# Kernel optimization log

Hardware: AMD Instinct MI355X
Metric: run time of the kernel (lower is better)

Reference implementation:

```python
import math
import jax, jax.numpy as jnp
import numpy as np

B, T, D_MODEL, H, D = 2, 1024, 1024, 16, 64
NUM_LEVELS = int(math.ceil(math.log2(T + 1))) + 1  # 12 for max_seq_len=1024


def _fenwick_level(idx):
    return (idx & -idx).bit_length() - 1


def build_fenwick_masks(T, num_levels):
    """NumPy replica of the torch build_fenwick_masks; returns [L, T, T] float32."""
    j_to_nodes = {}
    for j in range(1, T + 1):
        nodes = []
        idx = j
        while idx <= T:
            nodes.append((idx, _fenwick_level(idx)))
            idx += idx & -idx
        j_to_nodes[j] = nodes
    t_to_query_nodes = {}
    for t in range(1, T + 1):
        s = set()
        idx = t
        while idx > 0:
            s.add(idx)
            idx -= idx & -idx
        t_to_query_nodes[t] = s
    masks = np.zeros((num_levels, T, T), dtype=np.float32)
    for t in range(1, T + 1):
        qn = t_to_query_nodes[t]
        for j in range(1, t + 1):
            for node_idx, node_level in j_to_nodes[j]:
                if node_idx in qn:
                    masks[min(node_level, num_levels - 1), t - 1, j - 1] = 1.0
                    break
    return masks


def setup_inputs() -> dict:
    key = jax.random.key(0)
    ks = jax.random.split(key, 8)
    s = 0.02
    return {
        "x": jax.random.normal(ks[0], (B, T, D_MODEL), jnp.float32),
        "qw": jax.random.normal(ks[1], (D_MODEL, H * D), jnp.float32) * s,
        "qb": jnp.zeros((H * D,), jnp.float32),
        "kw": jax.random.normal(ks[2], (D_MODEL, H * D), jnp.float32) * s,
        "kb": jnp.zeros((H * D,), jnp.float32),
        "vw": jax.random.normal(ks[3], (D_MODEL, H * D), jnp.float32) * s,
        "vb": jnp.zeros((H * D,), jnp.float32),
        "lw": jax.random.normal(ks[4], (D_MODEL, H * NUM_LEVELS), jnp.float32) * s,
        "lb": jnp.zeros((H * NUM_LEVELS,), jnp.float32),
        "ow": jax.random.normal(ks[5], (H * D, D_MODEL), jnp.float32) * s,
        "ob": jnp.zeros((D_MODEL,), jnp.float32),
        "level_masks": jnp.asarray(build_fenwick_masks(T, NUM_LEVELS)),
    }


def reference(x, qw, qb, kw, kb, vw, vb, lw, lb, ow, ob, level_masks):
    b, t, _ = x.shape
    phi = lambda a: jax.nn.elu(a) + 1.0  # ELU+1 feature map
    # projections -> [B, H, T, D]
    Q = (x @ qw + qb).reshape(b, t, H, D).transpose(0, 2, 1, 3)
    K = (x @ kw + kb).reshape(b, t, H, D).transpose(0, 2, 1, 3)
    V = (x @ vw + vb).reshape(b, t, H, D).transpose(0, 2, 1, 3)
    Qp, Kp = phi(Q), phi(K)
    # per-level mixing weights: [B, H, T, L]
    logits = (x @ lw + lb).reshape(b, t, H, NUM_LEVELS).transpose(0, 2, 1, 3)
    w = jax.nn.softmax(logits, axis=-1)
    # scores are level-independent in the original; compute once
    S = jnp.einsum('bhid,bhjd->bhij', Qp, Kp)
    # sum_l w_l * mask_l folded into one weighted mask: [B, H, T, T]
    Mw = jnp.einsum('bhil,lij->bhij', w, level_masks)
    Sm = S * Mw
    num = jnp.einsum('bhij,bhjd->bhid', Sm, V)
    den = jnp.maximum(jnp.sum(Sm, axis=-1, keepdims=True), 1e-6)
    out = (num / den).transpose(0, 2, 1, 3).reshape(b, t, H * D)
    return out @ ow + ob
```

## Files before the change

### kernel.cpp

```cpp
#include <hip/hip_runtime.h>
#include <math.h>

typedef __bf16 bf16;
typedef __attribute__((ext_vector_type(8))) __bf16 bf16x8;
typedef __attribute__((ext_vector_type(4))) float f32x4;

#define B_SZ 2
#define T_SZ 1024
#define DM_SZ 1024
#define H_SZ 16
#define D_SZ 64
#define L_SZ 12
#define M_ROWS 2048
#define N_FUSED 3264

__device__ __forceinline__ f32x4 mfma_16x16x32(bf16x8 a, bf16x8 b, f32x4 c) {
  return __builtin_amdgcn_mfma_f32_16x16x32_bf16(a, b, c, 0, 0, 0);
}

__global__ __launch_bounds__(256) void k_cast(const float* __restrict__ in,
                                              bf16* __restrict__ out) {
  const int idx = blockIdx.x * 256 + threadIdx.x;
  const float* p = in + (size_t)idx * 8;
  f32x4 a = *(const f32x4*)p;
  f32x4 b = *(const f32x4*)(p + 4);
  bf16x8 o;
#pragma unroll
  for (int e = 0; e < 4; ++e) { o[e] = (bf16)a[e]; o[e + 4] = (bf16)b[e]; }
  *(bf16x8*)(out + (size_t)idx * 8) = o;
}

__global__ __launch_bounds__(256) void k_transpose4(
    const float* __restrict__ in0, bf16* __restrict__ out0,
    const float* __restrict__ in1, bf16* __restrict__ out1,
    const float* __restrict__ in2, bf16* __restrict__ out2,
    const float* __restrict__ in3, bf16* __restrict__ out3, int R, int C) {
  __shared__ __align__(16) bf16 tile[64][66];
  const float* in = blockIdx.z == 0 ? in0 : blockIdx.z == 1 ? in1 : blockIdx.z == 2 ? in2 : in3;
  bf16* out = blockIdx.z == 0 ? out0 : blockIdx.z == 1 ? out1 : blockIdx.z == 2 ? out2 : out3;
  const int tc = blockIdx.x * 64;
  const int tr = blockIdx.y * 64;
  const int t = threadIdx.x;
  const int r = t >> 2;
  const int c4 = (t & 3) << 4;
  const float* src = in + (size_t)(tr + r) * C + tc + c4;
  f32x4 f0 = *(const f32x4*)(src);
  f32x4 f1 = *(const f32x4*)(src + 4);
  f32x4 f2 = *(const f32x4*)(src + 8);
  f32x4 f3 = *(const f32x4*)(src + 12);
#pragma unroll
  for (int e = 0; e < 4; ++e) {
    tile[r][c4 + e]      = (bf16)f0[e];
    tile[r][c4 + 4 + e]  = (bf16)f1[e];
    tile[r][c4 + 8 + e]  = (bf16)f2[e];
    tile[r][c4 + 12 + e] = (bf16)f3[e];
  }
  __syncthreads();
  bf16x8 w0, w1;
#pragma unroll
  for (int e = 0; e < 8; ++e) { w0[e] = tile[c4 + e][r]; w1[e] = tile[c4 + 8 + e][r]; }
  bf16* dst = out + (size_t)(tc + r) * R + tr + c4;
  *(bf16x8*)(dst) = w0;
  *(bf16x8*)(dst + 8) = w1;
}

__global__ __launch_bounds__(256) void k_vtrans(const bf16* __restrict__ V,
                                                bf16* __restrict__ VTg) {
  __shared__ __align__(16) bf16 tile[64][66];
  const int tt = blockIdx.x;
  const int bh = blockIdx.y;
  const int b = bh >> 4, h = bh & 15;
  const int t0 = tt * 64;
  const int t = threadIdx.x;
  const int r = t >> 2;
  const int c4 = (t & 3) << 4;
  const bf16* src = V + (size_t)(b * T_SZ + t0 + r) * DM_SZ + h * 64 + c4;
  bf16x8 v0 = *(const bf16x8*)(src);
  bf16x8 v1 = *(const bf16x8*)(src + 8);
#pragma unroll
  for (int e = 0; e < 8; ++e) { tile[r][c4 + e] = v0[e]; tile[r][c4 + 8 + e] = v1[e]; }
  __syncthreads();
  bf16x8 w0, w1;
#pragma unroll
  for (int e = 0; e < 8; ++e) { w0[e] = tile[c4 + e][r]; w1[e] = tile[c4 + 8 + e][r]; }
  bf16* dst = VTg + ((size_t)bh * 64 + r) * T_SZ + t0 + c4;
  *(bf16x8*)(dst) = w0;
  *(bf16x8*)(dst + 8) = w1;
}

__global__ __launch_bounds__(256) void k_gemm_qkvl(
    const bf16* __restrict__ A, const bf16* __restrict__ Wt,
    const float* __restrict__ qb, const float* __restrict__ kb,
    const float* __restrict__ vb, const float* __restrict__ lb,
    bf16* __restrict__ Qp, bf16* __restrict__ Kp, bf16* __restrict__ V,
    float* __restrict__ logit) {
  __shared__ __align__(16) bf16 As[128][80];
  __shared__ __align__(16) bf16 Bs[64][80];
  const int nb = blockIdx.x * 64;
  const int mb = blockIdx.y * 128;
  const int t = threadIdx.x;
  const int wv = t >> 6;
  const int lane = t & 63;
  const int l16 = lane & 15;
  const int quad = lane >> 4;
  const int m0 = wv * 32;

  const int ar = t >> 1;
  const int ak = (t & 1) << 5;
  const int br = t >> 2;
  const int bk = (t & 3) << 4;

  const f32x4 zero4 = {0.f, 0.f, 0.f, 0.f};
  f32x4 acc[2][4];
#pragma unroll
  for (int i = 0; i < 2; ++i)
#pragma unroll
    for (int j = 0; j < 4; ++j) acc[i][j] = zero4;

  for (int k0 = 0; k0 < DM_SZ; k0 += 64) {
    const bf16* apg = A + (size_t)(mb + ar) * DM_SZ + k0 + ak;
    bf16x8 a0 = *(const bf16x8*)(apg);
    bf16x8 a1 = *(const bf16x8*)(apg + 8);
    bf16x8 a2 = *(const bf16x8*)(apg + 16);
    bf16x8 a3 = *(const bf16x8*)(apg + 24);
    const bf16* bpg = Wt + (size_t)(nb + br) * DM_SZ + k0 + bk;
    bf16x8 b0 = *(const bf16x8*)(bpg);
    bf16x8 b1 = *(const bf16x8*)(bpg + 8);
    __syncthreads();
    *(bf16x8*)&As[ar][ak] = a0;
    *(bf16x8*)&As[ar][ak + 8] = a1;
    *(bf16x8*)&As[ar][ak + 16] = a2;
    *(bf16x8*)&As[ar][ak + 24] = a3;
    *(bf16x8*)&Bs[br][bk] = b0;
    *(bf16x8*)&Bs[br][bk + 8] = b1;
    __syncthreads();
#pragma unroll
    for (int ks = 0; ks < 2; ++ks) {
      bf16x8 af0 = *(const bf16x8*)&As[m0 + l16][ks * 32 + quad * 8];
      bf16x8 af1 = *(const bf16x8*)&As[m0 + 16 + l16][ks * 32 + quad * 8];
#pragma unroll
      for (int tn = 0; tn < 4; ++tn) {
        bf16x8 bfr = *(const bf16x8*)&Bs[tn * 16 + l16][ks * 32 + quad * 8];
        acc[0][tn] = mfma_16x16x32(af0, bfr, acc[0][tn]);
        acc[1][tn] = mfma_16x16x32(af1, bfr, acc[1][tn]);
      }
    }
  }

  const int seg = nb >> 10;
  const int colseg0 = nb - (seg << 10);
  const float* bias = seg == 0 ? qb : seg == 1 ? kb : seg == 2 ? vb : lb;
  bf16* outb = seg == 0 ? Qp : seg == 1 ? Kp : V;

#pragma unroll
  for (int mi = 0; mi < 2; ++mi) {
#pragma unroll
    for (int tn = 0; tn < 4; ++tn) {
      const int col = colseg0 + tn * 16 + l16;
      const float bv = bias[col];
#pragma unroll
      for (int r = 0; r < 4; ++r) {
        const int row = mb + m0 + mi * 16 + quad * 4 + r;
        float v = acc[mi][tn][r] + bv;
        if (seg == 3) {
          logit[(size_t)row * (H_SZ * L_SZ) + col] = v;
        } else {
          if (seg < 2) v = (v > 0.f) ? (v + 1.f) : __expf(v);
          outb[(size_t)row * DM_SZ + col] = (bf16)v;
        }
      }
    }
  }
}

__global__ __launch_bounds__(256) void k_softmax12(float* __restrict__ lg, int n) {
  const int idx = blockIdx.x * 256 + threadIdx.x;
  if (idx >= n) return;
  float* p = lg + (size_t)idx * L_SZ;
  float m = p[0];
#pragma unroll
  for (int l = 1; l < L_SZ; ++l) m = fmaxf(m, p[l]);
  float e[L_SZ], s = 0.f;
#pragma unroll
  for (int l = 0; l < L_SZ; ++l) { e[l] = __expf(p[l] - m); s += e[l]; }
  const float inv = 1.f / s;
#pragma unroll
  for (int l = 0; l < L_SZ; ++l) p[l] = e[l] * inv;
}

__global__ __launch_bounds__(256) void k_attn(const bf16* __restrict__ Qp,
                                              const bf16* __restrict__ Kp,
                                              const bf16* __restrict__ VTg,
                                              const float* __restrict__ W,
                                              bf16* __restrict__ O) {
  __shared__ __align__(16) bf16 Ks[64][80];
  __shared__ __align__(16) bf16 VTs[64][80];
  __shared__ __align__(16) bf16 Pl[4][16][80];
  __shared__ float Ws[64 * L_SZ];

  const int idx = blockIdx.x;
  const int s = idx >> 5;
  const int bh = idx & 31;
  const int it = (s < 8) ? (15 - s) : (s - 8);
  const int b = bh >> 4;
  const int h = bh & 15;
  const int i0 = it * 64;
  const int t = threadIdx.x;
  const int wv = t >> 6;
  const int lane = t & 63;
  const int l16 = lane & 15;
  const int quad = lane >> 4;
  const int m0 = wv * 16;

  const size_t base_bt = (size_t)b * T_SZ;

  const bf16* qptr = Qp + (base_bt + i0 + m0 + l16) * DM_SZ + h * 64 + quad * 8;
  const bf16x8 aq0 = *(const bf16x8*)(qptr);
  const bf16x8 aq1 = *(const bf16x8*)(qptr + 32);

  {
    const int f = t * 3;
#pragma unroll
    for (int u = 0; u < 3; ++u) {
      const int ff = f + u;
      const int il = ff / L_SZ, l = ff % L_SZ;
      Ws[ff] = W[(base_bt + i0 + il) * (H_SZ * L_SZ) + h * L_SZ + l];
    }
  }

  const f32x4 zero4 = {0.f, 0.f, 0.f, 0.f};
  f32x4 accn[4];
#pragma unroll
  for (int tn = 0; tn < 4; ++tn) accn[tn] = zero4;
  float den[4] = {0.f, 0.f, 0.f, 0.f};

  const int sr = t >> 2;
  const int sc = (t & 3) << 4;

  const bf16* vtrow = VTg + ((size_t)bh * 64 + sr) * T_SZ;

  for (int jt = 0; jt <= it; ++jt) {
    const int j0 = jt * 64;
    const bf16* kpg = Kp + (base_bt + j0 + sr) * DM_SZ + h * 64 + sc;
    bf16x8 k0v = *(const bf16x8*)(kpg);
    bf16x8 k1v = *(const bf16x8*)(kpg + 8);
    const bf16* vpg = vtrow + j0 + sc;
    bf16x8 v0v = *(const bf16x8*)(vpg);
    bf16x8 v1v = *(const bf16x8*)(vpg + 8);
    __syncthreads();
    *(bf16x8*)&Ks[sr][sc] = k0v;
    *(bf16x8*)&Ks[sr][sc + 8] = k1v;
    *(bf16x8*)&VTs[sr][sc] = v0v;
    *(bf16x8*)&VTs[sr][sc + 8] = v1v;
    __syncthreads();

    f32x4 sacc[4];
#pragma unroll
    for (int tn = 0; tn < 4; ++tn) {
      sacc[tn] = zero4;
      bf16x8 bk0 = *(const bf16x8*)&Ks[tn * 16 + l16][quad * 8];
      bf16x8 bk1 = *(const bf16x8*)&Ks[tn * 16 + l16][32 + quad * 8];
      sacc[tn] = mfma_16x16x32(aq0, bk0, sacc[tn]);
      sacc[tn] = mfma_16x16x32(aq1, bk1, sacc[tn]);
    }

#pragma unroll
    for (int tn = 0; tn < 4; ++tn) {
#pragma unroll
      for (int r = 0; r < 4; ++r) {
        const int il = m0 + quad * 4 + r;
        const int ig = i0 + il;
        const int jg = j0 + tn * 16 + l16;
        float p = 0.f;
        if (jg <= ig) {
          const int lvl = 31 - __clz((unsigned)((ig + 1) ^ jg));
          p = sacc[tn][r] * Ws[il * L_SZ + lvl];
        }
        den[r] += p;
        Pl[wv][quad * 4 + r][(tn * 16 + l16) ^ (quad << 4)] = (bf16)p;
      }
    }

#pragma unroll
    for (int ks = 0; ks < 2; ++ks) {
      bf16x8 apf = *(const bf16x8*)&Pl[wv][l16][(ks * 32 + quad * 8) ^ ((l16 >> 2) << 4)];
#pragma unroll
      for (int tn = 0; tn < 4; ++tn) {
        bf16x8 bvf = *(const bf16x8*)&VTs[tn * 16 + l16][ks * 32 + quad * 8];
        accn[tn] = mfma_16x16x32(apf, bvf, accn[tn]);
      }
    }
  }

#pragma unroll
  for (int r = 0; r < 4; ++r) {
    float d = den[r];
    d += __shfl_xor(d, 1, 64);
    d += __shfl_xor(d, 2, 64);
    d += __shfl_xor(d, 4, 64);
    d += __shfl_xor(d, 8, 64);
    den[r] = fmaxf(d, 1e-6f);
  }

#pragma unroll
  for (int tn = 0; tn < 4; ++tn) {
#pragma unroll
    for (int r = 0; r < 4; ++r) {
      const int il = m0 + quad * 4 + r;
      O[(base_bt + i0 + il) * DM_SZ + h * 64 + tn * 16 + l16] =
          (bf16)(accn[tn][r] / den[r]);
    }
  }
}

__global__ __launch_bounds__(256) void k_gemm_out(const bf16* __restrict__ A,
                                                  const bf16* __restrict__ Wt,
                                                  const float* __restrict__ bias,
                                                  float* __restrict__ out) {
  __shared__ __align__(16) bf16 As[64][80];
  __shared__ __align__(16) bf16 Bs[64][80];
  const int nb = blockIdx.x * 64;
  const int mb = blockIdx.y * 64;
  const int t = threadIdx.x;
  const int wv = t >> 6;
  const int lane = t & 63;
  const int l16 = lane & 15;
  const int quad = lane >> 4;

  const int sr = t >> 2;
  const int sc = (t & 3) << 4;

  const f32x4 zero4 = {0.f, 0.f, 0.f, 0.f};
  f32x4 acc[4];
#pragma unroll
  for (int j = 0; j < 4; ++j) acc[j] = zero4;

  for (int k0 = 0; k0 < DM_SZ; k0 += 64) {
    const bf16* apg = A + (size_t)(mb + sr) * DM_SZ + k0 + sc;
    bf16x8 a0 = *(const bf16x8*)(apg);
    bf16x8 a1 = *(const bf16x8*)(apg + 8);
    const bf16* bpg = Wt + (size_t)(nb + sr) * DM_SZ + k0 + sc;
    bf16x8 b0 = *(const bf16x8*)(bpg);
    bf16x8 b1 = *(const bf16x8*)(bpg + 8);
    __syncthreads();
    *(bf16x8*)&As[sr][sc] = a0;
    *(bf16x8*)&As[sr][sc + 8] = a1;
    *(bf16x8*)&Bs[sr][sc] = b0;
    *(bf16x8*)&Bs[sr][sc + 8] = b1;
    __syncthreads();
#pragma unroll
    for (int ks = 0; ks < 2; ++ks) {
      bf16x8 af = *(const bf16x8*)&As[wv * 16 + l16][ks * 32 + quad * 8];
#pragma unroll
      for (int tn = 0; tn < 4; ++tn) {
        bf16x8 bfr = *(const bf16x8*)&Bs[tn * 16 + l16][ks * 32 + quad * 8];
        acc[tn] = mfma_16x16x32(af, bfr, acc[tn]);
      }
    }
  }
#pragma unroll
  for (int tn = 0; tn < 4; ++tn) {
    const int col = nb + tn * 16 + l16;
    const float bv = bias[col];
#pragma unroll
    for (int r = 0; r < 4; ++r) {
      const int row = mb + wv * 16 + quad * 4 + r;
      out[(size_t)row * DM_SZ + col] = acc[tn][r] + bv;
    }
  }
}

extern "C" void kernel_launch(void* const* d_in, const int* in_sizes, int n_in,
                              void* d_out, int out_size, void* d_ws, size_t ws_size,
                              hipStream_t stream) {
  (void)in_sizes; (void)n_in; (void)out_size; (void)ws_size;
  const float* x  = (const float*)d_in[0];
  const float* qw = (const float*)d_in[1];
  const float* qb = (const float*)d_in[2];
  const float* kw = (const float*)d_in[3];
  const float* kb = (const float*)d_in[4];
  const float* vw = (const float*)d_in[5];
  const float* vb = (const float*)d_in[6];
  const float* lw = (const float*)d_in[7];
  const float* lb = (const float*)d_in[8];
  const float* ow = (const float*)d_in[9];
  const float* ob = (const float*)d_in[10];

  char* ws = (char*)d_ws;
  size_t off = 0;
  auto alloc = [&](size_t bytes) -> char* {
    char* p = ws + off;
    off += (bytes + 255) & ~(size_t)255;
    return p;
  };
  bf16* xb     = (bf16*)alloc((size_t)M_ROWS * DM_SZ * 2);
  bf16* wqkvlT = (bf16*)alloc((size_t)N_FUSED * DM_SZ * 2);
  bf16* owT    = (bf16*)alloc((size_t)DM_SZ * DM_SZ * 2);
  bf16* Qp     = (bf16*)alloc((size_t)M_ROWS * DM_SZ * 2);
  bf16* Kpb    = (bf16*)alloc((size_t)M_ROWS * DM_SZ * 2);
  bf16* Vb     = (bf16*)alloc((size_t)M_ROWS * DM_SZ * 2);
  bf16* VTg    = (bf16*)alloc((size_t)M_ROWS * DM_SZ * 2);
  bf16* attn   = (bf16*)alloc((size_t)M_ROWS * DM_SZ * 2);
  float* logit = (float*)alloc((size_t)M_ROWS * H_SZ * L_SZ * 4);

  const dim3 blk(256);
  k_cast<<<dim3(M_ROWS * DM_SZ / 8 / 256), blk, 0, stream>>>(x, xb);
  k_transpose4<<<dim3(16, 16, 4), blk, 0, stream>>>(
      qw, wqkvlT, kw, wqkvlT + (size_t)1024 * DM_SZ, vw, wqkvlT + (size_t)2048 * DM_SZ,
      ow, owT, DM_SZ, DM_SZ);
  k_transpose4<<<dim3(3, 16, 1), blk, 0, stream>>>(
      lw, wqkvlT + (size_t)3072 * DM_SZ, lw, nullptr, lw, nullptr, lw, nullptr,
      DM_SZ, H_SZ * L_SZ);

  k_gemm_qkvl<<<dim3(N_FUSED / 64, M_ROWS / 128), blk, 0, stream>>>(
      xb, wqkvlT, qb, kb, vb, lb, Qp, Kpb, Vb, logit);

  k_softmax12<<<dim3((M_ROWS * H_SZ) / 256), blk, 0, stream>>>(logit, M_ROWS * H_SZ);
  k_vtrans<<<dim3(T_SZ / 64, B_SZ * H_SZ), blk, 0, stream>>>(Vb, VTg);

  k_attn<<<dim3((T_SZ / 64) * B_SZ * H_SZ), blk, 0, stream>>>(Qp, Kpb, VTg, logit, attn);

  k_gemm_out<<<dim3(DM_SZ / 64, M_ROWS / 64), blk, 0, stream>>>(attn, owT, ob, (float*)d_out);
}
```

Baseline: 202.0 us.

## Use 128-wide direct-to-LDS GEMMs, split logit GEMM, fuse softmax into attention

Replaces the QKV and output projection GEMMs with a templated 128-column-tile GEMM. It loads tiles straight into LDS through global_load_lds, which removes register staging and the padded LDS layout. The logit projection moves to its own small GEMM, and the level softmax is computed inside the attention kernel, so the separate softmax launch is dropped. The weight transposes are merged into a single launch. The unpadded LDS layout may cause bank conflicts, and each block still loads once per k-step with no double buffering.

```diff
diff --git a/kernel.cpp b/kernel.cpp
--- a/kernel.cpp
+++ b/kernel.cpp
@@ -12,10 +12,16 @@
 #define D_SZ 64
 #define L_SZ 12
 #define M_ROWS 2048
-#define N_FUSED 3264
+#define N_QKV 3072
 
 __device__ __forceinline__ f32x4 mfma_16x16x32(bf16x8 a, bf16x8 b, f32x4 c) {
   return __builtin_amdgcn_mfma_f32_16x16x32_bf16(a, b, c, 0, 0, 0);
+}
+
+__device__ __forceinline__ void gload_lds16(const bf16* g, bf16* l) {
+  __builtin_amdgcn_global_load_lds((const __attribute__((address_space(1))) void*)g,
+                                   (__attribute__((address_space(3))) void*)l,
+                                   16, 0, 0);
 }
 
 __global__ __launch_bounds__(256) void k_cast(const float* __restrict__ in,
@@ -30,14 +36,21 @@
   *(bf16x8*)(out + (size_t)idx * 8) = o;
 }
 
-__global__ __launch_bounds__(256) void k_transpose4(
+__global__ __launch_bounds__(256) void k_transpose5(
     const float* __restrict__ in0, bf16* __restrict__ out0,
     const float* __restrict__ in1, bf16* __restrict__ out1,
     const float* __restrict__ in2, bf16* __restrict__ out2,
-    const float* __restrict__ in3, bf16* __restrict__ out3, int R, int C) {
+    const float* __restrict__ in3, bf16* __restrict__ out3,
+    const float* __restrict__ in4, bf16* __restrict__ out4) {
   __shared__ __align__(16) bf16 tile[64][66];
-  const float* in = blockIdx.z == 0 ? in0 : blockIdx.z == 1 ? in1 : blockIdx.z == 2 ? in2 : in3;
-  bf16* out = blockIdx.z == 0 ? out0 : blockIdx.z == 1 ? out1 : blockIdx.z == 2 ? out2 : out3;
+  const int z = blockIdx.z;
+  const float* in; bf16* out; int C = 1024;
+  if (z == 0)      { in = in0; out = out0; }
+  else if (z == 1) { in = in1; out = out1; }
+  else if (z == 2) { in = in2; out = out2; }
+  else if (z == 3) { in = in3; out = out3; }
+  else             { in = in4; out = out4; C = 192; if (blockIdx.x >= 3) return; }
+  const int R = 1024;
   const int tc = blockIdx.x * 64;
   const int tr = blockIdx.y * 64;
   const int t = threadIdx.x;
@@ -88,12 +101,105 @@
   *(bf16x8*)(dst + 8) = w1;
 }
 
-__global__ __launch_bounds__(256) void k_gemm_qkvl(
+template <int TM, int EPI>
+__global__ __launch_bounds__(256) void k_gemm128(
     const bf16* __restrict__ A, const bf16* __restrict__ Wt,
     const float* __restrict__ qb, const float* __restrict__ kb,
-    const float* __restrict__ vb, const float* __restrict__ lb,
+    const float* __restrict__ vb,
     bf16* __restrict__ Qp, bf16* __restrict__ Kp, bf16* __restrict__ V,
-    float* __restrict__ logit) {
+    float* __restrict__ outF) {
+  constexpr int MI = TM / 32;
+  __shared__ __align__(16) bf16 As[TM * 64];
+  __shared__ __align__(16) bf16 Bs[128 * 64];
+  const int nb = blockIdx.x * 128;
+  const int mb = blockIdx.y * TM;
+  const int t = threadIdx.x;
+  const int wv = t >> 6;
+  const int lane = t & 63;
+  const int l16 = lane & 15;
+  const int quad = lane >> 4;
+  const int wm = (wv & 1) * (TM / 2);
+  const int wn = (wv >> 1) * 64;
+
+  const int trow = t >> 3;
+  const int tcol = (t & 7) * 8;
+
+  const f32x4 zero4 = {0.f, 0.f, 0.f, 0.f};
+  f32x4 acc[MI][4];
+#pragma unroll
+  for (int i = 0; i < MI; ++i)
+#pragma unroll
+    for (int j = 0; j < 4; ++j) acc[i][j] = zero4;
+
+  const bf16* ag = A + (size_t)(mb + trow) * DM_SZ + tcol;
+  const bf16* bg = Wt + (size_t)(nb + trow) * DM_SZ + tcol;
+
+  for (int k0 = 0; k0 < DM_SZ; k0 += 64) {
+    __syncthreads();
+#pragma unroll
+    for (int i = 0; i < MI; ++i)
+      gload_lds16(ag + (size_t)i * 32 * DM_SZ + k0, As + i * 2048 + t * 8);
+#pragma unroll
+    for (int i = 0; i < 4; ++i)
+      gload_lds16(bg + (size_t)i * 32 * DM_SZ + k0, Bs + i * 2048 + t * 8);
+    __syncthreads();
+#pragma unroll
+    for (int ks = 0; ks < 2; ++ks) {
+      bf16x8 af[MI];
+#pragma unroll
+      for (int mi = 0; mi < MI; ++mi)
+        af[mi] = *(const bf16x8*)(As + (wm + mi * 16 + l16) * 64 + ks * 32 + quad * 8);
+#pragma unroll
+      for (int ni = 0; ni < 4; ++ni) {
+        bf16x8 bfr = *(const bf16x8*)(Bs + (wn + ni * 16 + l16) * 64 + ks * 32 + quad * 8);
+#pragma unroll
+        for (int mi = 0; mi < MI; ++mi)
+          acc[mi][ni] = mfma_16x16x32(af[mi], bfr, acc[mi][ni]);
+      }
+    }
+  }
+
+  if (EPI == 0) {
+    const int seg = nb >> 10;
+    const int c0 = (nb & 1023) + wn;
+    const float* bias = seg == 0 ? qb : seg == 1 ? kb : vb;
+    bf16* outp = seg == 0 ? Qp : seg == 1 ? Kp : V;
+#pragma unroll
+    for (int ni = 0; ni < 4; ++ni) {
+      const int col = c0 + ni * 16 + l16;
+      const float bv = bias[col];
+#pragma unroll
+      for (int mi = 0; mi < MI; ++mi) {
+#pragma unroll
+        for (int r = 0; r < 4; ++r) {
+          const int row = mb + wm + mi * 16 + quad * 4 + r;
+          float v = acc[mi][ni][r] + bv;
+          if (seg < 2) v = (v > 0.f) ? (v + 1.f) : __expf(v);
+          outp[(size_t)row * DM_SZ + col] = (bf16)v;
+        }
+      }
+    }
+  } else {
+#pragma unroll
+    for (int ni = 0; ni < 4; ++ni) {
+      const int col = nb + wn + ni * 16 + l16;
+      const float bv = qb[col];
+#pragma unroll
+      for (int mi = 0; mi < MI; ++mi) {
+#pragma unroll
+        for (int r = 0; r < 4; ++r) {
+          const int row = mb + wm + mi * 16 + quad * 4 + r;
+          outF[(size_t)row * DM_SZ + col] = acc[mi][ni][r] + bv;
+        }
+      }
+    }
+  }
+}
+
+__global__ __launch_bounds__(256) void k_gemm_logit(const bf16* __restrict__ A,
+                                                    const bf16* __restrict__ Wt,
+                                                    const float* __restrict__ lb,
+                                                    float* __restrict__ logit) {
   __shared__ __align__(16) bf16 As[128][80];
   __shared__ __align__(16) bf16 Bs[64][80];
   const int nb = blockIdx.x * 64;
@@ -146,52 +252,25 @@
       }
     }
   }
-
-  const int seg = nb >> 10;
-  const int colseg0 = nb - (seg << 10);
-  const float* bias = seg == 0 ? qb : seg == 1 ? kb : seg == 2 ? vb : lb;
-  bf16* outb = seg == 0 ? Qp : seg == 1 ? Kp : V;
-
 #pragma unroll
   for (int mi = 0; mi < 2; ++mi) {
 #pragma unroll
     for (int tn = 0; tn < 4; ++tn) {
-      const int col = colseg0 + tn * 16 + l16;
-      const float bv = bias[col];
+      const int col = nb + tn * 16 + l16;
+      const float bv = lb[col];
 #pragma unroll
       for (int r = 0; r < 4; ++r) {
         const int row = mb + m0 + mi * 16 + quad * 4 + r;
-        float v = acc[mi][tn][r] + bv;
-        if (seg == 3) {
-          logit[(size_t)row * (H_SZ * L_SZ) + col] = v;
-        } else {
-          if (seg < 2) v = (v > 0.f) ? (v + 1.f) : __expf(v);
-          outb[(size_t)row * DM_SZ + col] = (bf16)v;
-        }
-      }
-    }
-  }
-}
-
-__global__ __launch_bounds__(256) void k_softmax12(float* __restrict__ lg, int n) {
-  const int idx = blockIdx.x * 256 + threadIdx.x;
-  if (idx >= n) return;
-  float* p = lg + (size_t)idx * L_SZ;
-  float m = p[0];
-#pragma unroll
-  for (int l = 1; l < L_SZ; ++l) m = fmaxf(m, p[l]);
-  float e[L_SZ], s = 0.f;
-#pragma unroll
-  for (int l = 0; l < L_SZ; ++l) { e[l] = __expf(p[l] - m); s += e[l]; }
-  const float inv = 1.f / s;
-#pragma unroll
-  for (int l = 0; l < L_SZ; ++l) p[l] = e[l] * inv;
+        logit[(size_t)row * (H_SZ * L_SZ) + col] = acc[mi][tn][r] + bv;
+      }
+    }
+  }
 }
 
 __global__ __launch_bounds__(256) void k_attn(const bf16* __restrict__ Qp,
                                               const bf16* __restrict__ Kp,
                                               const bf16* __restrict__ VTg,
-                                              const float* __restrict__ W,
+                                              const float* __restrict__ Lg,
                                               bf16* __restrict__ O) {
   __shared__ __align__(16) bf16 Ks[64][80];
   __shared__ __align__(16) bf16 VTs[64][80];
@@ -218,14 +297,18 @@
   const bf16x8 aq0 = *(const bf16x8*)(qptr);
   const bf16x8 aq1 = *(const bf16x8*)(qptr + 32);
 
-  {
-    const int f = t * 3;
-#pragma unroll
-    for (int u = 0; u < 3; ++u) {
-      const int ff = f + u;
-      const int il = ff / L_SZ, l = ff % L_SZ;
-      Ws[ff] = W[(base_bt + i0 + il) * (H_SZ * L_SZ) + h * L_SZ + l];
-    }
+  if (t < 64) {
+    const float* lp = Lg + (base_bt + i0 + t) * (H_SZ * L_SZ) + h * L_SZ;
+    float v[L_SZ];
+    float m = -1e30f;
+#pragma unroll
+    for (int l = 0; l < L_SZ; ++l) { v[l] = lp[l]; m = fmaxf(m, v[l]); }
+    float sum = 0.f;
+#pragma unroll
+    for (int l = 0; l < L_SZ; ++l) { v[l] = __expf(v[l] - m); sum += v[l]; }
+    const float inv = 1.f / sum;
+#pragma unroll
+    for (int l = 0; l < L_SZ; ++l) Ws[t * L_SZ + l] = v[l] * inv;
   }
 
   const f32x4 zero4 = {0.f, 0.f, 0.f, 0.f};
@@ -309,63 +392,6 @@
       const int il = m0 + quad * 4 + r;
       O[(base_bt + i0 + il) * DM_SZ + h * 64 + tn * 16 + l16] =
           (bf16)(accn[tn][r] / den[r]);
-    }
-  }
-}
-
-__global__ __launch_bounds__(256) void k_gemm_out(const bf16* __restrict__ A,
-                                                  const bf16* __restrict__ Wt,
-                                                  const float* __restrict__ bias,
-                                                  float* __restrict__ out) {
-  __shared__ __align__(16) bf16 As[64][80];
-  __shared__ __align__(16) bf16 Bs[64][80];
-  const int nb = blockIdx.x * 64;
-  const int mb = blockIdx.y * 64;
-  const int t = threadIdx.x;
-  const int wv = t >> 6;
-  const int lane = t & 63;
-  const int l16 = lane & 15;
-  const int quad = lane >> 4;
-
-  const int sr = t >> 2;
-  const int sc = (t & 3) << 4;
-
-  const f32x4 zero4 = {0.f, 0.f, 0.f, 0.f};
-  f32x4 acc[4];
-#pragma unroll
-  for (int j = 0; j < 4; ++j) acc[j] = zero4;
-
-  for (int k0 = 0; k0 < DM_SZ; k0 += 64) {
-    const bf16* apg = A + (size_t)(mb + sr) * DM_SZ + k0 + sc;
-    bf16x8 a0 = *(const bf16x8*)(apg);
-    bf16x8 a1 = *(const bf16x8*)(apg + 8);
-    const bf16* bpg = Wt + (size_t)(nb + sr) * DM_SZ + k0 + sc;
-    bf16x8 b0 = *(const bf16x8*)(bpg);
-    bf16x8 b1 = *(const bf16x8*)(bpg + 8);
-    __syncthreads();
-    *(bf16x8*)&As[sr][sc] = a0;
-    *(bf16x8*)&As[sr][sc + 8] = a1;
-    *(bf16x8*)&Bs[sr][sc] = b0;
-    *(bf16x8*)&Bs[sr][sc + 8] = b1;
-    __syncthreads();
-#pragma unroll
-    for (int ks = 0; ks < 2; ++ks) {
-      bf16x8 af = *(const bf16x8*)&As[wv * 16 + l16][ks * 32 + quad * 8];
-#pragma unroll
-      for (int tn = 0; tn < 4; ++tn) {
-        bf16x8 bfr = *(const bf16x8*)&Bs[tn * 16 + l16][ks * 32 + quad * 8];
-        acc[tn] = mfma_16x16x32(af, bfr, acc[tn]);
-      }
-    }
-  }
-#pragma unroll
-  for (int tn = 0; tn < 4; ++tn) {
-    const int col = nb + tn * 16 + l16;
-    const float bv = bias[col];
-#pragma unroll
-    for (int r = 0; r < 4; ++r) {
-      const int row = mb + wv * 16 + quad * 4 + r;
-      out[(size_t)row * DM_SZ + col] = acc[tn][r] + bv;
     }
   }
 }
@@ -394,7 +420,8 @@
     return p;
   };
   bf16* xb     = (bf16*)alloc((size_t)M_ROWS * DM_SZ * 2);
-  bf16* wqkvlT = (bf16*)alloc((size_t)N_FUSED * DM_SZ * 2);
+  bf16* wqkvT  = (bf16*)alloc((size_t)N_QKV * DM_SZ * 2);
+  bf16* lwT    = (bf16*)alloc((size_t)(H_SZ * L_SZ) * DM_SZ * 2);
   bf16* owT    = (bf16*)alloc((size_t)DM_SZ * DM_SZ * 2);
   bf16* Qp     = (bf16*)alloc((size_t)M_ROWS * DM_SZ * 2);
   bf16* Kpb    = (bf16*)alloc((size_t)M_ROWS * DM_SZ * 2);
@@ -405,20 +432,21 @@
 
   const dim3 blk(256);
   k_cast<<<dim3(M_ROWS * DM_SZ / 8 / 256), blk, 0, stream>>>(x, xb);
-  k_transpose4<<<dim3(16, 16, 4), blk, 0, stream>>>(
-      qw, wqkvlT, kw, wqkvlT + (size_t)1024 * DM_SZ, vw, wqkvlT + (size_t)2048 * DM_SZ,
-      ow, owT, DM_SZ, DM_SZ);
-  k_transpose4<<<dim3(3, 16, 1), blk, 0, stream>>>(
-      lw, wqkvlT + (size_t)3072 * DM_SZ, lw, nullptr, lw, nullptr, lw, nullptr,
-      DM_SZ, H_SZ * L_SZ);
-
-  k_gemm_qkvl<<<dim3(N_FUSED / 64, M_ROWS / 128), blk, 0, stream>>>(
-      xb, wqkvlT, qb, kb, vb, lb, Qp, Kpb, Vb, logit);
-
-  k_softmax12<<<dim3((M_ROWS * H_SZ) / 256), blk, 0, stream>>>(logit, M_ROWS * H_SZ);
+  k_transpose5<<<dim3(16, 16, 5), blk, 0, stream>>>(
+      qw, wqkvT,
+      kw, wqkvT + (size_t)1024 * DM_SZ,
+      vw, wqkvT + (size_t)2048 * DM_SZ,
+      ow, owT,
+      lw, lwT);
+
+  k_gemm128<128, 0><<<dim3(N_QKV / 128, M_ROWS / 128), blk, 0, stream>>>(
+      xb, wqkvT, qb, kb, vb, Qp, Kpb, Vb, nullptr);
+  k_gemm_logit<<<dim3(3, 16), blk, 0, stream>>>(xb, lwT, lb, logit);
+
   k_vtrans<<<dim3(T_SZ / 64, B_SZ * H_SZ), blk, 0, stream>>>(Vb, VTg);
 
   k_attn<<<dim3((T_SZ / 64) * B_SZ * H_SZ), blk, 0, stream>>>(Qp, Kpb, VTg, logit, attn);
 
-  k_gemm_out<<<dim3(DM_SZ / 64, M_ROWS / 64), blk, 0, stream>>>(attn, owT, ob, (float*)d_out);
-}
+  k_gemm128<64, 1><<<dim3(DM_SZ / 128, M_ROWS / 64), blk, 0, stream>>>(
+      attn, owT, ob, nullptr, nullptr, nullptr, nullptr, nullptr, (float*)d_out);
+}
```

Result: slower. 218.5 us (+8.1%).
